# Kernel tuning notes

Hardware: AMD Instinct MI355X
Metric: run time of the kernel (lower is better)

The kernel has to match this reference:

```python
import jax, jax.numpy as jnp
import numpy as np

E = 1024
H = 8
D = E // H
B = 16384
LN_EPS = 1e-5


def setup_inputs() -> dict:
    key = jax.random.key(0)
    ks = jax.random.split(key, 12)
    s = 1.0 / np.sqrt(E)
    return {
        "image_features": jax.random.normal(ks[0], (B, E), jnp.float32),
        "signal_features": jax.random.normal(ks[1], (B, E), jnp.float32),
        "Wq": jax.random.normal(ks[2], (E, E), jnp.float32) * s,
        "Wk": jax.random.normal(ks[3], (E, E), jnp.float32) * s,
        "Wv": jax.random.normal(ks[4], (E, E), jnp.float32) * s,
        "bq": jnp.zeros((E,), jnp.float32),
        "bk": jnp.zeros((E,), jnp.float32),
        "bv": jnp.zeros((E,), jnp.float32),
        "Wo": jax.random.normal(ks[5], (E, E), jnp.float32) * s,
        "bo": jnp.zeros((E,), jnp.float32),
        "ln_gamma": jnp.ones((E,), jnp.float32),
        "ln_beta": jnp.zeros((E,), jnp.float32),
    }


def _forward(image_features, signal_features, Wq, Wk, Wv, bq, bk, bv, Wo, bo, ln_gamma, ln_beta):
    # query: [B,1,E] from image; key/value: [B,2,E] stacked modalities
    kv = jnp.stack([image_features, signal_features], axis=1)  # [B,2,E]
    # projections (torch Linear convention: x @ W^T + b)
    q = (image_features @ Wq.T + bq).reshape(B, H, 1, D)       # [B,H,1,D]
    k = (kv @ Wk.T + bk).reshape(B, 2, H, D).transpose(0, 2, 1, 3)  # [B,H,2,D]
    v = (kv @ Wv.T + bv).reshape(B, 2, H, D).transpose(0, 2, 1, 3)  # [B,H,2,D]
    scale = 1.0 / jnp.sqrt(jnp.float32(D))
    scores = jnp.einsum("bhqd,bhkd->bhqk", q, k) * scale       # [B,H,1,2]
    attn = jax.nn.softmax(scores, axis=-1)
    ctx = jnp.einsum("bhqk,bhkd->bhqd", attn, v)               # [B,H,1,D]
    ctx = ctx.reshape(B, E)
    attn_out = ctx @ Wo.T + bo
    # residual + LayerNorm (dropout is identity in eval)
    fused = attn_out + image_features
    mu = jnp.mean(fused, axis=-1, keepdims=True)
    var = jnp.var(fused, axis=-1, keepdims=True)
    normed = (fused - mu) * jax.lax.rsqrt(var + LN_EPS)
    return normed * ln_gamma + ln_beta


def reference(image_features, signal_features, Wq, Wk, Wv, bq, bk, bv, Wo, bo, ln_gamma, ln_beta):
    return _forward(image_features, signal_features, Wq, Wk, Wv, bq, bk, bv, Wo, bo, ln_gamma, ln_beta)
```

## Files before the change

### kernel.cpp

```cpp
#include <hip/hip_runtime.h>

#define B_ 16384
#define E_ 1024
#define H_ 8
#define D_ 128
#define BK 32

typedef _Float16 f16;
typedef _Float16 f16x8 __attribute__((ext_vector_type(8)));
typedef float f32x4 __attribute__((ext_vector_type(4)));

__device__ __forceinline__ void gload16(const f16* g, f16* l) {
    __builtin_amdgcn_global_load_lds(
        (const __attribute__((address_space(1))) void*)g,
        (__attribute__((address_space(3))) void*)l, 16, 0, 0);
}

__global__ __launch_bounds__(256) void cvt_kernel(const float4* __restrict__ src,
                                                  ushort4* __restrict__ dst, int n4) {
    int i = blockIdx.x * 256 + threadIdx.x;
    if (i >= n4) return;
    float4 v = src[i];
    union { ushort4 u; f16 h[4]; } o;
    o.h[0] = (f16)v.x; o.h[1] = (f16)v.y; o.h[2] = (f16)v.z; o.h[3] = (f16)v.w;
    dst[i] = o.u;
}

__global__ __launch_bounds__(256, 2) void qkv_attn_kernel(
    const f16* __restrict__ Xi, const f16* __restrict__ Xs,
    const f16* __restrict__ Wq, const f16* __restrict__ Wk, const f16* __restrict__ Wv,
    const float* __restrict__ bq, const float* __restrict__ bk, const float* __restrict__ bv,
    f16* __restrict__ ctx)
{
    __shared__ f16 sAi[64][BK];
    __shared__ f16 sAs[64][BK];
    __shared__ f16 sWq[128][BK];
    __shared__ f16 sWk[128][BK];
    __shared__ f16 sWv[128][BK];
    __shared__ float sdot[2][64][2];
    __shared__ float sa0[64];

    const int tid  = threadIdx.x;
    const int lane = tid & 63;
    const int wave = tid >> 6;
    const int wr = wave >> 1, wc = wave & 1;
    const int l16 = lane & 15, lq = lane >> 4;

    const int row0 = blockIdx.x * 64;
    const int col0 = blockIdx.y * D_;

    const int lr = lane >> 2;
    const int lc = (lane & 3) * 8;

    const f16* gAi = Xi + (size_t)(row0 + wave * 16 + lr) * E_ + lc;
    const f16* gAs = Xs + (size_t)(row0 + wave * 16 + lr) * E_ + lc;
    const size_t woff = (size_t)(col0 + wave * 32 + lr) * E_ + lc;
    const f16* gWq = Wq + woff;
    const f16* gWk = Wk + woff;
    const f16* gWv = Wv + woff;
    const size_t wskip = (size_t)16 * E_;

    f16* lAi  = &sAi[wave * 16][0];
    f16* lAs  = &sAs[wave * 16][0];
    f16* lWq0 = &sWq[wave * 32][0];      f16* lWq1 = &sWq[wave * 32 + 16][0];
    f16* lWk0 = &sWk[wave * 32][0];      f16* lWk1 = &sWk[wave * 32 + 16][0];
    f16* lWv0 = &sWv[wave * 32][0];      f16* lWv1 = &sWv[wave * 32 + 16][0];

    f32x4 zero4 = {0.f, 0.f, 0.f, 0.f};
    f32x4 accQ[2][4], accKi[2][4], accKs[2][4], accVi[2][4], accVs[2][4];
    #pragma unroll
    for (int i = 0; i < 2; i++)
        #pragma unroll
        for (int j = 0; j < 4; j++) {
            accQ[i][j] = zero4; accKi[i][j] = zero4; accKs[i][j] = zero4;
            accVi[i][j] = zero4; accVs[i][j] = zero4;
        }

    for (int kk = 0; kk < E_; kk += BK) {
        gload16(gAi + kk, lAi);
        gload16(gAs + kk, lAs);
        gload16(gWq + kk, lWq0);
        gload16(gWq + wskip + kk, lWq1);
        gload16(gWk + kk, lWk0);
        gload16(gWk + wskip + kk, lWk1);
        gload16(gWv + kk, lWv0);
        gload16(gWv + wskip + kk, lWv1);
        __syncthreads();

        f16x8 aI[2], aS[2], bF[4];
        #pragma unroll
        for (int fr = 0; fr < 2; fr++) {
            aI[fr] = *(const f16x8*)&sAi[wr * 32 + fr * 16 + l16][lq * 8];
            aS[fr] = *(const f16x8*)&sAs[wr * 32 + fr * 16 + l16][lq * 8];
        }
        #pragma unroll
        for (int fc = 0; fc < 4; fc++)
            bF[fc] = *(const f16x8*)&sWq[wc * 64 + fc * 16 + l16][lq * 8];
        #pragma unroll
        for (int fr = 0; fr < 2; fr++)
            #pragma unroll
            for (int fc = 0; fc < 4; fc++)
                accQ[fr][fc] = __builtin_amdgcn_mfma_f32_16x16x32_f16(aI[fr], bF[fc], accQ[fr][fc], 0, 0, 0);
        #pragma unroll
        for (int fc = 0; fc < 4; fc++)
            bF[fc] = *(const f16x8*)&sWk[wc * 64 + fc * 16 + l16][lq * 8];
        #pragma unroll
        for (int fr = 0; fr < 2; fr++)
            #pragma unroll
            for (int fc = 0; fc < 4; fc++) {
                accKi[fr][fc] = __builtin_amdgcn_mfma_f32_16x16x32_f16(aI[fr], bF[fc], accKi[fr][fc], 0, 0, 0);
                accKs[fr][fc] = __builtin_amdgcn_mfma_f32_16x16x32_f16(aS[fr], bF[fc], accKs[fr][fc], 0, 0, 0);
            }
        #pragma unroll
        for (int fc = 0; fc < 4; fc++)
            bF[fc] = *(const f16x8*)&sWv[wc * 64 + fc * 16 + l16][lq * 8];
        #pragma unroll
        for (int fr = 0; fr < 2; fr++)
            #pragma unroll
            for (int fc = 0; fc < 4; fc++) {
                accVi[fr][fc] = __builtin_amdgcn_mfma_f32_16x16x32_f16(aI[fr], bF[fc], accVi[fr][fc], 0, 0, 0);
                accVs[fr][fc] = __builtin_amdgcn_mfma_f32_16x16x32_f16(aS[fr], bF[fc], accVs[fr][fc], 0, 0, 0);
            }
        __syncthreads();
    }

    #pragma unroll
    for (int fc = 0; fc < 4; fc++) {
        int col = col0 + wc * 64 + fc * 16 + l16;
        float bqv = bq[col], bkv = bk[col];
        #pragma unroll
        for (int fr = 0; fr < 2; fr++)
            #pragma unroll
            for (int e = 0; e < 4; e++) {
                accQ[fr][fc][e]  += bqv;
                accKi[fr][fc][e] += bkv;
                accKs[fr][fc][e] += bkv;
            }
    }

    #pragma unroll
    for (int fr = 0; fr < 2; fr++)
        #pragma unroll
        for (int e = 0; e < 4; e++) {
            float d0 = 0.f, d1 = 0.f;
            #pragma unroll
            for (int fc = 0; fc < 4; fc++) {
                d0 += accQ[fr][fc][e] * accKi[fr][fc][e];
                d1 += accQ[fr][fc][e] * accKs[fr][fc][e];
            }
            #pragma unroll
            for (int m = 1; m < 16; m <<= 1) {
                d0 += __shfl_xor(d0, m, 64);
                d1 += __shfl_xor(d1, m, 64);
            }
            if (l16 == 0) {
                int row = wr * 32 + fr * 16 + lq * 4 + e;
                sdot[0][row][wc] = d0;
                sdot[1][row][wc] = d1;
            }
        }
    __syncthreads();
    if (tid < 64) {
        const float scale = 0.088388347648318447f;
        float s0 = (sdot[0][tid][0] + sdot[0][tid][1]) * scale;
        float s1 = (sdot[1][tid][0] + sdot[1][tid][1]) * scale;
        sa0[tid] = 1.0f / (1.0f + expf(s1 - s0));
    }
    __syncthreads();

    #pragma unroll
    for (int fc = 0; fc < 4; fc++) {
        int col = col0 + wc * 64 + fc * 16 + l16;
        float bvv = bv[col];
        #pragma unroll
        for (int fr = 0; fr < 2; fr++)
            #pragma unroll
            for (int e = 0; e < 4; e++) {
                int row = wr * 32 + fr * 16 + lq * 4 + e;
                float a0 = sa0[row];
                float v  = a0 * accVi[fr][fc][e] + (1.0f - a0) * accVs[fr][fc][e] + bvv;
                ctx[(size_t)(row0 + row) * E_ + col] = (f16)v;
            }
    }
}

__global__ __launch_bounds__(256) void out_proj_kernel(
    const f16* __restrict__ A, const f16* __restrict__ Wo, const float* __restrict__ bo,
    const float* __restrict__ resid, float* __restrict__ out)
{
    __shared__ f16 sA[128][BK];
    __shared__ f16 sB[128][BK];
    const int tid  = threadIdx.x;
    const int lane = tid & 63;
    const int wave = tid >> 6;
    const int wr = wave >> 1, wc = wave & 1;
    const int l16 = lane & 15, lq = lane >> 4;
    const int row0 = blockIdx.x * 128;
    const int col0 = blockIdx.y * 128;

    const int lr = lane >> 2;
    const int lc = (lane & 3) * 8;
    const f16* gA0 = A  + (size_t)(row0 + wave * 32 + lr) * E_ + lc;
    const f16* gB0 = Wo + (size_t)(col0 + wave * 32 + lr) * E_ + lc;
    const size_t wskip = (size_t)16 * E_;
    f16* lA0 = &sA[wave * 32][0];      f16* lA1 = &sA[wave * 32 + 16][0];
    f16* lB0 = &sB[wave * 32][0];      f16* lB1 = &sB[wave * 32 + 16][0];

    f32x4 zero4 = {0.f, 0.f, 0.f, 0.f};
    f32x4 acc[4][4];
    #pragma unroll
    for (int i = 0; i < 4; i++)
        #pragma unroll
        for (int j = 0; j < 4; j++) acc[i][j] = zero4;

    for (int kk = 0; kk < E_; kk += BK) {
        gload16(gA0 + kk, lA0);
        gload16(gA0 + wskip + kk, lA1);
        gload16(gB0 + kk, lB0);
        gload16(gB0 + wskip + kk, lB1);
        __syncthreads();

        f16x8 aF[4], bF[4];
        #pragma unroll
        for (int f = 0; f < 4; f++) {
            aF[f] = *(const f16x8*)&sA[wr * 64 + f * 16 + l16][lq * 8];
            bF[f] = *(const f16x8*)&sB[wc * 64 + f * 16 + l16][lq * 8];
        }
        #pragma unroll
        for (int fr = 0; fr < 4; fr++)
            #pragma unroll
            for (int fc = 0; fc < 4; fc++)
                acc[fr][fc] = __builtin_amdgcn_mfma_f32_16x16x32_f16(aF[fr], bF[fc], acc[fr][fc], 0, 0, 0);
        __syncthreads();
    }

    #pragma unroll
    for (int fc = 0; fc < 4; fc++) {
        int col = col0 + wc * 64 + fc * 16 + l16;
        float bov = bo[col];
        #pragma unroll
        for (int fr = 0; fr < 4; fr++)
            #pragma unroll
            for (int e = 0; e < 4; e++) {
                int row = row0 + wr * 64 + fr * 16 + lq * 4 + e;
                out[(size_t)row * E_ + col] = acc[fr][fc][e] + bov + resid[(size_t)row * E_ + col];
            }
    }
}

__global__ __launch_bounds__(256) void ln_kernel(
    float* __restrict__ x, const float* __restrict__ gamma,
    const float* __restrict__ beta, float* __restrict__ out)
{
    const int row = blockIdx.x;
    const int tid = threadIdx.x;
    const float4* xr = (const float4*)(x + (size_t)row * E_);
    float4 v = xr[tid];
    float s  = v.x + v.y + v.z + v.w;
    float s2 = v.x * v.x + v.y * v.y + v.z * v.z + v.w * v.w;
    #pragma unroll
    for (int m = 1; m < 64; m <<= 1) {
        s  += __shfl_xor(s, m, 64);
        s2 += __shfl_xor(s2, m, 64);
    }
    __shared__ float red[8];
    int wv = tid >> 6, ln = tid & 63;
    if (ln == 0) { red[wv] = s; red[4 + wv] = s2; }
    __syncthreads();
    s  = red[0] + red[1] + red[2] + red[3];
    s2 = red[4] + red[5] + red[6] + red[7];
    float mu  = s * (1.0f / E_);
    float var = s2 * (1.0f / E_) - mu * mu;
    float r   = rsqrtf(var + 1e-5f);
    float4 g  = ((const float4*)gamma)[tid];
    float4 bb = ((const float4*)beta)[tid];
    float4 o;
    o.x = (v.x - mu) * r * g.x + bb.x;
    o.y = (v.y - mu) * r * g.y + bb.y;
    o.z = (v.z - mu) * r * g.z + bb.z;
    o.w = (v.w - mu) * r * g.w + bb.w;
    ((float4*)(out + (size_t)row * E_))[tid] = o;
}

extern "C" void kernel_launch(void* const* d_in, const int* in_sizes, int n_in,
                              void* d_out, int out_size, void* d_ws, size_t ws_size,
                              hipStream_t stream)
{
    (void)in_sizes; (void)n_in; (void)out_size; (void)ws_size;
    const float* image  = (const float*)d_in[0];
    const float* signal = (const float*)d_in[1];
    const float* Wq = (const float*)d_in[2];
    const float* Wk = (const float*)d_in[3];
    const float* Wv = (const float*)d_in[4];
    const float* bq = (const float*)d_in[5];
    const float* bk = (const float*)d_in[6];
    const float* bv = (const float*)d_in[7];
    const float* Wo = (const float*)d_in[8];
    const float* bo = (const float*)d_in[9];
    const float* gamma = (const float*)d_in[10];
    const float* beta  = (const float*)d_in[11];
    float* out = (float*)d_out;

    char* ws = (char*)d_ws;
    f16* Xi16 = (f16*)(ws);
    f16* Xs16 = (f16*)(ws + 32ull * 1024 * 1024);
    f16* Wq16 = (f16*)(ws + 64ull * 1024 * 1024);
    f16* Wk16 = (f16*)(ws + 66ull * 1024 * 1024);
    f16* Wv16 = (f16*)(ws + 68ull * 1024 * 1024);
    f16* Wo16 = (f16*)(ws + 70ull * 1024 * 1024);
    f16* ctx  = (f16*)(ws + 72ull * 1024 * 1024);

    const int nBE4 = B_ * E_ / 4;
    const int nEE4 = E_ * E_ / 4;
    cvt_kernel<<<nBE4 / 256, 256, 0, stream>>>((const float4*)image,  (ushort4*)Xi16, nBE4);
    cvt_kernel<<<nBE4 / 256, 256, 0, stream>>>((const float4*)signal, (ushort4*)Xs16, nBE4);
    cvt_kernel<<<nEE4 / 256, 256, 0, stream>>>((const float4*)Wq, (ushort4*)Wq16, nEE4);
    cvt_kernel<<<nEE4 / 256, 256, 0, stream>>>((const float4*)Wk, (ushort4*)Wk16, nEE4);
    cvt_kernel<<<nEE4 / 256, 256, 0, stream>>>((const float4*)Wv, (ushort4*)Wv16, nEE4);
    cvt_kernel<<<nEE4 / 256, 256, 0, stream>>>((const float4*)Wo, (ushort4*)Wo16, nEE4);

    dim3 g2(B_ / 64, H_);
    qkv_attn_kernel<<<g2, 256, 0, stream>>>(Xi16, Xs16, Wq16, Wk16, Wv16, bq, bk, bv, ctx);

    dim3 g4(B_ / 128, E_ / 128);
    out_proj_kernel<<<g4, 256, 0, stream>>>(ctx, Wo16, bo, image, out);

    ln_kernel<<<B_, 256, 0, stream>>>(out, gamma, beta, out);
}
```

Baseline: 481.7 us.

## Swizzle LDS tiles, double-buffer out-projection GEMM, and batch fp16 conversion launches

Both GEMM kernels now store and read their LDS tiles with an XOR column swizzle, meant to remove the bank conflicts caused by reading 16-byte fragments from rows with a 64-byte stride. The output-projection kernel gains a two-buffer LDS pipeline, so the next K-slice is loaded while MFMAs run on the current one, at the cost of twice the shared memory. The six fp32-to-fp16 conversion launches are merged into two grid-indexed launches to cut launch overhead. Correctness of the pipeline depends on the trailing barrier also waiting for the async global-to-LDS loads.

```diff
diff --git a/kernel.cpp b/kernel.cpp
--- a/kernel.cpp
+++ b/kernel.cpp
@@ -16,14 +16,39 @@
         (__attribute__((address_space(3))) void*)l, 16, 0, 0);
 }
 
-__global__ __launch_bounds__(256) void cvt_kernel(const float4* __restrict__ src,
-                                                  ushort4* __restrict__ dst, int n4) {
+
+__global__ __launch_bounds__(256) void cvt2_kernel(const float4* __restrict__ s0,
+                                                   const float4* __restrict__ s1,
+                                                   ushort4* __restrict__ d0,
+                                                   ushort4* __restrict__ d1, int n4) {
+    const float4* s = blockIdx.y ? s1 : s0;
+    ushort4* d = blockIdx.y ? d1 : d0;
     int i = blockIdx.x * 256 + threadIdx.x;
     if (i >= n4) return;
-    float4 v = src[i];
+    float4 v = s[i];
     union { ushort4 u; f16 h[4]; } o;
     o.h[0] = (f16)v.x; o.h[1] = (f16)v.y; o.h[2] = (f16)v.z; o.h[3] = (f16)v.w;
-    dst[i] = o.u;
+    d[i] = o.u;
+}
+
+__global__ __launch_bounds__(256) void cvt4_kernel(
+    const float4* __restrict__ s0, const float4* __restrict__ s1,
+    const float4* __restrict__ s2, const float4* __restrict__ s3,
+    ushort4* __restrict__ d0, ushort4* __restrict__ d1,
+    ushort4* __restrict__ d2, ushort4* __restrict__ d3, int n4) {
+    const float4* s; ushort4* d;
+    switch (blockIdx.y) {
+        case 0: s = s0; d = d0; break;
+        case 1: s = s1; d = d1; break;
+        case 2: s = s2; d = d2; break;
+        default: s = s3; d = d3; break;
+    }
+    int i = blockIdx.x * 256 + threadIdx.x;
+    if (i >= n4) return;
+    float4 v = s[i];
+    union { ushort4 u; f16 h[4]; } o;
+    o.h[0] = (f16)v.x; o.h[1] = (f16)v.y; o.h[2] = (f16)v.z; o.h[3] = (f16)v.w;
+    d[i] = o.u;
 }
 
 __global__ __launch_bounds__(256, 2) void qkv_attn_kernel(
@@ -50,7 +75,8 @@
     const int col0 = blockIdx.y * D_;
 
     const int lr = lane >> 2;
-    const int lc = (lane & 3) * 8;
+    const int lc = ((lane & 3) ^ ((lane >> 3) & 3)) * 8;
+    const int rc = (lq ^ ((l16 >> 1) & 3)) * 8;
 
     const f16* gAi = Xi + (size_t)(row0 + wave * 16 + lr) * E_ + lc;
     const f16* gAs = Xs + (size_t)(row0 + wave * 16 + lr) * E_ + lc;
@@ -90,12 +116,12 @@
         f16x8 aI[2], aS[2], bF[4];
         #pragma unroll
         for (int fr = 0; fr < 2; fr++) {
-            aI[fr] = *(const f16x8*)&sAi[wr * 32 + fr * 16 + l16][lq * 8];
-            aS[fr] = *(const f16x8*)&sAs[wr * 32 + fr * 16 + l16][lq * 8];
+            aI[fr] = *(const f16x8*)&sAi[wr * 32 + fr * 16 + l16][rc];
+            aS[fr] = *(const f16x8*)&sAs[wr * 32 + fr * 16 + l16][rc];
         }
         #pragma unroll
         for (int fc = 0; fc < 4; fc++)
-            bF[fc] = *(const f16x8*)&sWq[wc * 64 + fc * 16 + l16][lq * 8];
+            bF[fc] = *(const f16x8*)&sWq[wc * 64 + fc * 16 + l16][rc];
         #pragma unroll
         for (int fr = 0; fr < 2; fr++)
             #pragma unroll
@@ -103,7 +129,7 @@
                 accQ[fr][fc] = __builtin_amdgcn_mfma_f32_16x16x32_f16(aI[fr], bF[fc], accQ[fr][fc], 0, 0, 0);
         #pragma unroll
         for (int fc = 0; fc < 4; fc++)
-            bF[fc] = *(const f16x8*)&sWk[wc * 64 + fc * 16 + l16][lq * 8];
+            bF[fc] = *(const f16x8*)&sWk[wc * 64 + fc * 16 + l16][rc];
         #pragma unroll
         for (int fr = 0; fr < 2; fr++)
             #pragma unroll
@@ -113,7 +139,7 @@
             }
         #pragma unroll
         for (int fc = 0; fc < 4; fc++)
-            bF[fc] = *(const f16x8*)&sWv[wc * 64 + fc * 16 + l16][lq * 8];
+            bF[fc] = *(const f16x8*)&sWv[wc * 64 + fc * 16 + l16][rc];
         #pragma unroll
         for (int fr = 0; fr < 2; fr++)
             #pragma unroll
@@ -188,8 +214,8 @@
     const f16* __restrict__ A, const f16* __restrict__ Wo, const float* __restrict__ bo,
     const float* __restrict__ resid, float* __restrict__ out)
 {
-    __shared__ f16 sA[128][BK];
-    __shared__ f16 sB[128][BK];
+    __shared__ f16 sA[2][128][BK];
+    __shared__ f16 sB[2][128][BK];
     const int tid  = threadIdx.x;
     const int lane = tid & 63;
     const int wave = tid >> 6;
@@ -199,12 +225,12 @@
     const int col0 = blockIdx.y * 128;
 
     const int lr = lane >> 2;
-    const int lc = (lane & 3) * 8;
+    const int lc = ((lane & 3) ^ ((lane >> 3) & 3)) * 8;
+    const int rc = (lq ^ ((l16 >> 1) & 3)) * 8;
+
     const f16* gA0 = A  + (size_t)(row0 + wave * 32 + lr) * E_ + lc;
     const f16* gB0 = Wo + (size_t)(col0 + wave * 32 + lr) * E_ + lc;
     const size_t wskip = (size_t)16 * E_;
-    f16* lA0 = &sA[wave * 32][0];      f16* lA1 = &sA[wave * 32 + 16][0];
-    f16* lB0 = &sB[wave * 32][0];      f16* lB1 = &sB[wave * 32 + 16][0];
 
     f32x4 zero4 = {0.f, 0.f, 0.f, 0.f};
     f32x4 acc[4][4];
@@ -213,18 +239,26 @@
         #pragma unroll
         for (int j = 0; j < 4; j++) acc[i][j] = zero4;
 
-    for (int kk = 0; kk < E_; kk += BK) {
-        gload16(gA0 + kk, lA0);
-        gload16(gA0 + wskip + kk, lA1);
-        gload16(gB0 + kk, lB0);
-        gload16(gB0 + wskip + kk, lB1);
-        __syncthreads();
+    auto stage = [&](int buf, int kk) {
+        gload16(gA0 + kk,         &sA[buf][wave * 32][0]);
+        gload16(gA0 + wskip + kk, &sA[buf][wave * 32 + 16][0]);
+        gload16(gB0 + kk,         &sB[buf][wave * 32][0]);
+        gload16(gB0 + wskip + kk, &sB[buf][wave * 32 + 16][0]);
+    };
+
+    stage(0, 0);
+    __syncthreads();
+
+    const int NT = E_ / BK;
+    for (int t = 0; t < NT; ++t) {
+        const int cur = t & 1;
+        if (t + 1 < NT) stage(cur ^ 1, (t + 1) * BK);
 
         f16x8 aF[4], bF[4];
         #pragma unroll
         for (int f = 0; f < 4; f++) {
-            aF[f] = *(const f16x8*)&sA[wr * 64 + f * 16 + l16][lq * 8];
-            bF[f] = *(const f16x8*)&sB[wc * 64 + f * 16 + l16][lq * 8];
+            aF[f] = *(const f16x8*)&sA[cur][wr * 64 + f * 16 + l16][rc];
+            bF[f] = *(const f16x8*)&sB[cur][wc * 64 + f * 16 + l16][rc];
         }
         #pragma unroll
         for (int fr = 0; fr < 4; fr++)
@@ -312,12 +346,14 @@
 
     const int nBE4 = B_ * E_ / 4;
     const int nEE4 = E_ * E_ / 4;
-    cvt_kernel<<<nBE4 / 256, 256, 0, stream>>>((const float4*)image,  (ushort4*)Xi16, nBE4);
-    cvt_kernel<<<nBE4 / 256, 256, 0, stream>>>((const float4*)signal, (ushort4*)Xs16, nBE4);
-    cvt_kernel<<<nEE4 / 256, 256, 0, stream>>>((const float4*)Wq, (ushort4*)Wq16, nEE4);
-    cvt_kernel<<<nEE4 / 256, 256, 0, stream>>>((const float4*)Wk, (ushort4*)Wk16, nEE4);
-    cvt_kernel<<<nEE4 / 256, 256, 0, stream>>>((const float4*)Wv, (ushort4*)Wv16, nEE4);
-    cvt_kernel<<<nEE4 / 256, 256, 0, stream>>>((const float4*)Wo, (ushort4*)Wo16, nEE4);
+    dim3 gX(nBE4 / 256, 2);
+    cvt2_kernel<<<gX, 256, 0, stream>>>((const float4*)image, (const float4*)signal,
+                                        (ushort4*)Xi16, (ushort4*)Xs16, nBE4);
+    dim3 gW(nEE4 / 256, 4);
+    cvt4_kernel<<<gW, 256, 0, stream>>>((const float4*)Wq, (const float4*)Wk,
+                                        (const float4*)Wv, (const float4*)Wo,
+                                        (ushort4*)Wq16, (ushort4*)Wk16,
+                                        (ushort4*)Wv16, (ushort4*)Wo16, nEE4);
 
     dim3 g2(B_ / 64, H_);
     qkv_attn_kernel<<<g2, 256, 0, stream>>>(Xi16, Xs16, Wq16, Wk16, Wv16, bq, bk, bv, ctx);
```

New measurement: 470.3 us. 1.02x faster.
